# Kernel optimization log

Hardware: AMD Instinct MI355X
Metric: run time of the kernel (lower is better)

The kernel has to match this reference:

```python
import jax, jax.numpy as jnp
import numpy as np

B = 32768
F = 256
H1 = 16
H2 = 8

def setup_inputs() -> dict:
    key = jax.random.key(0)
    ks = jax.random.split(key, 9)
    x = jax.random.normal(ks[0], (B, F), dtype=jnp.float32)
    # Stacked per-feature MLP params (one UnivariateNetwork per feature)
    W1 = jax.random.normal(ks[1], (F, H1), dtype=jnp.float32) * (1.0 / np.sqrt(1))
    b1 = jax.random.normal(ks[2], (F, H1), dtype=jnp.float32) * 0.05
    W2 = jax.random.normal(ks[3], (F, H1, H2), dtype=jnp.float32) * (1.0 / np.sqrt(H1))
    b2 = jax.random.normal(ks[4], (F, H2), dtype=jnp.float32) * 0.05
    W3 = jax.random.normal(ks[5], (F, H2), dtype=jnp.float32) * (1.0 / np.sqrt(H2))
    b3 = jax.random.normal(ks[6], (F,), dtype=jnp.float32) * 0.05
    theta = jax.random.uniform(ks[7], (F,), dtype=jnp.float32) * 0.05
    bias = jnp.zeros((1,), dtype=jnp.float32)
    return {"x": x, "W1": W1, "b1": b1, "W2": W2, "b2": b2,
            "W3": W3, "b3": b3, "theta": theta, "bias": bias}

def reference(x, W1, b1, W2, b2, W3, b3, theta, bias):
    # Batched per-feature MLP: 1 -> H1 -> H2 -> 1 with ELU, all features at once.
    h1 = jax.nn.elu(x[:, :, None] * W1[None, :, :] + b1[None, :, :])      # [B, F, H1]
    h2 = jax.nn.elu(jnp.einsum('bfh,fhk->bfk', h1, W2) + b2[None, :, :])  # [B, F, H2]
    Z = jnp.einsum('bfk,fk->bf', h2, W3) + b3[None, :]                    # [B, F]
    weights = jax.nn.softplus(theta)                                      # [F]
    y_pred = Z @ weights + bias                                           # [B]
    return (y_pred, weights, Z)
```

## Files before the change

kernel.cpp:

```cpp
#include <hip/hip_runtime.h>

#define NB 32768
#define NF 256
#define H1 16
#define H2 8
#define FG 16
#define RJ 4
#define ROWS_PER_BLOCK (16 * RJ)

__device__ __forceinline__ float elu_f(float v) {
    return v > 0.0f ? v : (__expf(v) - 1.0f);
}

__global__ __launch_bounds__(256)
void nul_init(const float* __restrict__ theta, const float* __restrict__ bias,
              float* __restrict__ y_out, float* __restrict__ w_out) {
    const int t = blockIdx.x * 256 + threadIdx.x;
    if (t < NB) y_out[t] = bias[0];
    if (t < NF) w_out[t] = __logf(1.0f + __expf(theta[t]));
}

__global__ __launch_bounds__(256)
void nul_main(const float* __restrict__ x,
              const float* __restrict__ W1, const float* __restrict__ b1,
              const float* __restrict__ W2, const float* __restrict__ b2,
              const float* __restrict__ W3, const float* __restrict__ b3,
              const float* __restrict__ theta,
              float* __restrict__ y_out, float* __restrict__ z_out) {
    __shared__ __align__(16) float sW1[FG][17];
    __shared__ __align__(16) float sB1[FG][17];
    __shared__ __align__(16) float sW2[FG][132];
    __shared__ __align__(16) float sB2[FG][12];
    __shared__ __align__(16) float sW3[FG][12];
    __shared__ float sB3[FG];
    __shared__ float sWv[FG];

    const int tid  = threadIdx.x;
    const int f0   = blockIdx.y * FG;
    const int row0 = blockIdx.x * ROWS_PER_BLOCK;

    {
        const int f = tid >> 4, h = tid & 15;
        sW1[f][h] = W1[(f0 + f) * H1 + h];
        sB1[f][h] = b1[(f0 + f) * H1 + h];
    }
    {
        const int e = tid * 8;
        const int ff = e >> 7, c = e & 127;
        const float4* p = reinterpret_cast<const float4*>(W2 + (f0 + ff) * (H1 * H2) + c);
        float4 v0 = p[0], v1 = p[1];
        float* d = &sW2[ff][c];
        d[0] = v0.x; d[1] = v0.y; d[2] = v0.z; d[3] = v0.w;
        d[4] = v1.x; d[5] = v1.y; d[6] = v1.z; d[7] = v1.w;
    }
    if (tid < FG * H2) {
        const int f = tid >> 3, k = tid & 7;
        sB2[f][k] = b2[(f0 + f) * H2 + k];
        sW3[f][k] = W3[(f0 + f) * H2 + k];
    }
    if (tid < FG) {
        sB3[tid] = b3[f0 + tid];
        sWv[tid] = __logf(1.0f + __expf(theta[f0 + tid]));
    }
    __syncthreads();

    const int fl = tid & 15;
    const int rl = tid >> 4;
    const int f  = f0 + fl;

    float xv[RJ];
    #pragma unroll
    for (int j = 0; j < RJ; ++j)
        xv[j] = x[(row0 + rl + 16 * j) * NF + f];

    float acc[RJ][H2];
    {
        const float4 ba = *reinterpret_cast<const float4*>(&sB2[fl][0]);
        const float4 bb = *reinterpret_cast<const float4*>(&sB2[fl][4]);
        #pragma unroll
        for (int j = 0; j < RJ; ++j) {
            acc[j][0] = ba.x; acc[j][1] = ba.y; acc[j][2] = ba.z; acc[j][3] = ba.w;
            acc[j][4] = bb.x; acc[j][5] = bb.y; acc[j][6] = bb.z; acc[j][7] = bb.w;
        }
    }

    #pragma unroll
    for (int hq = 0; hq < H1 / 4; ++hq) {
        const float4 w1q = *reinterpret_cast<const float4*>(&sW1[fl][hq * 4]);
        const float4 b1q = *reinterpret_cast<const float4*>(&sB1[fl][hq * 4]);
        const float w1a[4] = {w1q.x, w1q.y, w1q.z, w1q.w};
        const float b1a[4] = {b1q.x, b1q.y, b1q.z, b1q.w};
        #pragma unroll
        for (int hh = 0; hh < 4; ++hh) {
            const int h = hq * 4 + hh;
            const float4 wa = *reinterpret_cast<const float4*>(&sW2[fl][h * 8]);
            const float4 wb = *reinterpret_cast<const float4*>(&sW2[fl][h * 8 + 4]);
            #pragma unroll
            for (int j = 0; j < RJ; ++j) {
                const float h1 = elu_f(fmaf(xv[j], w1a[hh], b1a[hh]));
                acc[j][0] = fmaf(h1, wa.x, acc[j][0]);
                acc[j][1] = fmaf(h1, wa.y, acc[j][1]);
                acc[j][2] = fmaf(h1, wa.z, acc[j][2]);
                acc[j][3] = fmaf(h1, wa.w, acc[j][3]);
                acc[j][4] = fmaf(h1, wb.x, acc[j][4]);
                acc[j][5] = fmaf(h1, wb.y, acc[j][5]);
                acc[j][6] = fmaf(h1, wb.z, acc[j][6]);
                acc[j][7] = fmaf(h1, wb.w, acc[j][7]);
            }
        }
    }

    const float4 w3a = *reinterpret_cast<const float4*>(&sW3[fl][0]);
    const float4 w3b = *reinterpret_cast<const float4*>(&sW3[fl][4]);
    const float  b3v = sB3[fl];
    const float  wv  = sWv[fl];

    #pragma unroll
    for (int j = 0; j < RJ; ++j) {
        float z = b3v;
        z = fmaf(elu_f(acc[j][0]), w3a.x, z);
        z = fmaf(elu_f(acc[j][1]), w3a.y, z);
        z = fmaf(elu_f(acc[j][2]), w3a.z, z);
        z = fmaf(elu_f(acc[j][3]), w3a.w, z);
        z = fmaf(elu_f(acc[j][4]), w3b.x, z);
        z = fmaf(elu_f(acc[j][5]), w3b.y, z);
        z = fmaf(elu_f(acc[j][6]), w3b.z, z);
        z = fmaf(elu_f(acc[j][7]), w3b.w, z);

        const int row = row0 + rl + 16 * j;
        z_out[row * NF + f] = z;

        float p = wv * z;
        p += __shfl_xor(p, 1, 16);
        p += __shfl_xor(p, 2, 16);
        p += __shfl_xor(p, 4, 16);
        p += __shfl_xor(p, 8, 16);
        if (fl == 0) unsafeAtomicAdd(&y_out[row], p);
    }
}

extern "C" void kernel_launch(void* const* d_in, const int* in_sizes, int n_in,
                              void* d_out, int out_size, void* d_ws, size_t ws_size,
                              hipStream_t stream) {
    const float* x     = (const float*)d_in[0];
    const float* W1    = (const float*)d_in[1];
    const float* b1    = (const float*)d_in[2];
    const float* W2    = (const float*)d_in[3];
    const float* b2    = (const float*)d_in[4];
    const float* W3    = (const float*)d_in[5];
    const float* b3    = (const float*)d_in[6];
    const float* theta = (const float*)d_in[7];
    const float* bias  = (const float*)d_in[8];

    float* y_out = (float*)d_out;
    float* w_out = y_out + NB;
    float* z_out = w_out + NF;

    nul_init<<<NB / 256, 256, 0, stream>>>(theta, bias, y_out, w_out);

    dim3 grid(NB / ROWS_PER_BLOCK, NF / FG);
    nul_main<<<grid, 256, 0, stream>>>(
        x, W1, b1, W2, b2, W3, b3, theta, y_out, z_out);
}
```

Before: 161.4 us.

## Loop row chunks per block with x prefetch and ds_swizzle reductions

Each block now walks four chunks of 128 rows instead of handling 64 rows once. The x values for the next chunk are prefetched while the current chunk computes. This spreads the shared-memory weight staging over more rows and hides global-load latency. It doubles rows per thread per chunk, raising register pressure, and cuts the grid size by 8x. The shuffle-xor reduction is replaced with ds_swizzle xor patterns within 16-lane groups.

```diff
diff --git a/kernel.cpp b/kernel.cpp
--- a/kernel.cpp
+++ b/kernel.cpp
@@ -5,11 +5,18 @@
 #define H1 16
 #define H2 8
 #define FG 16
-#define RJ 4
-#define ROWS_PER_BLOCK (16 * RJ)
+#define RJ 8
+#define RT 4
+#define ROWS_PER_CHUNK (16 * RJ)
+#define ROWS_PER_BLOCK (ROWS_PER_CHUNK * RT)
 
 __device__ __forceinline__ float elu_f(float v) {
     return v > 0.0f ? v : (__expf(v) - 1.0f);
+}
+
+template <int PAT>
+__device__ __forceinline__ float swz_add(float p) {
+    return p + __int_as_float(__builtin_amdgcn_ds_swizzle(__float_as_int(p), PAT));
 }
 
 __global__ __launch_bounds__(256)
@@ -68,74 +75,90 @@
     const int rl = tid >> 4;
     const int f  = f0 + fl;
 
+    const float4 ba  = *reinterpret_cast<const float4*>(&sB2[fl][0]);
+    const float4 bb  = *reinterpret_cast<const float4*>(&sB2[fl][4]);
+    const float4 w3a = *reinterpret_cast<const float4*>(&sW3[fl][0]);
+    const float4 w3b = *reinterpret_cast<const float4*>(&sW3[fl][4]);
+    const float  b3v = sB3[fl];
+    const float  wv  = sWv[fl];
+    const float* xcol = x + f;
+
     float xv[RJ];
     #pragma unroll
     for (int j = 0; j < RJ; ++j)
-        xv[j] = x[(row0 + rl + 16 * j) * NF + f];
+        xv[j] = xcol[(row0 + rl + 16 * j) * NF];
 
-    float acc[RJ][H2];
-    {
-        const float4 ba = *reinterpret_cast<const float4*>(&sB2[fl][0]);
-        const float4 bb = *reinterpret_cast<const float4*>(&sB2[fl][4]);
+    #pragma unroll 1
+    for (int c = 0; c < RT; ++c) {
+        const int rbase = row0 + c * ROWS_PER_CHUNK;
+
+        float xn[RJ];
+        if (c + 1 < RT) {
+            #pragma unroll
+            for (int j = 0; j < RJ; ++j)
+                xn[j] = xcol[(rbase + ROWS_PER_CHUNK + rl + 16 * j) * NF];
+        }
+
+        float acc[RJ][H2];
         #pragma unroll
         for (int j = 0; j < RJ; ++j) {
             acc[j][0] = ba.x; acc[j][1] = ba.y; acc[j][2] = ba.z; acc[j][3] = ba.w;
             acc[j][4] = bb.x; acc[j][5] = bb.y; acc[j][6] = bb.z; acc[j][7] = bb.w;
         }
-    }
 
-    #pragma unroll
-    for (int hq = 0; hq < H1 / 4; ++hq) {
-        const float4 w1q = *reinterpret_cast<const float4*>(&sW1[fl][hq * 4]);
-        const float4 b1q = *reinterpret_cast<const float4*>(&sB1[fl][hq * 4]);
-        const float w1a[4] = {w1q.x, w1q.y, w1q.z, w1q.w};
-        const float b1a[4] = {b1q.x, b1q.y, b1q.z, b1q.w};
         #pragma unroll
-        for (int hh = 0; hh < 4; ++hh) {
-            const int h = hq * 4 + hh;
-            const float4 wa = *reinterpret_cast<const float4*>(&sW2[fl][h * 8]);
-            const float4 wb = *reinterpret_cast<const float4*>(&sW2[fl][h * 8 + 4]);
+        for (int hq = 0; hq < H1 / 4; ++hq) {
+            const float4 w1q = *reinterpret_cast<const float4*>(&sW1[fl][hq * 4]);
+            const float4 b1q = *reinterpret_cast<const float4*>(&sB1[fl][hq * 4]);
+            const float w1a[4] = {w1q.x, w1q.y, w1q.z, w1q.w};
+            const float b1a[4] = {b1q.x, b1q.y, b1q.z, b1q.w};
             #pragma unroll
-            for (int j = 0; j < RJ; ++j) {
-                const float h1 = elu_f(fmaf(xv[j], w1a[hh], b1a[hh]));
-                acc[j][0] = fmaf(h1, wa.x, acc[j][0]);
-                acc[j][1] = fmaf(h1, wa.y, acc[j][1]);
-                acc[j][2] = fmaf(h1, wa.z, acc[j][2]);
-                acc[j][3] = fmaf(h1, wa.w, acc[j][3]);
-                acc[j][4] = fmaf(h1, wb.x, acc[j][4]);
-                acc[j][5] = fmaf(h1, wb.y, acc[j][5]);
-                acc[j][6] = fmaf(h1, wb.z, acc[j][6]);
-                acc[j][7] = fmaf(h1, wb.w, acc[j][7]);
+            for (int hh = 0; hh < 4; ++hh) {
+                const int h = hq * 4 + hh;
+                const float4 wa = *reinterpret_cast<const float4*>(&sW2[fl][h * 8]);
+                const float4 wb = *reinterpret_cast<const float4*>(&sW2[fl][h * 8 + 4]);
+                #pragma unroll
+                for (int j = 0; j < RJ; ++j) {
+                    const float h1 = elu_f(fmaf(xv[j], w1a[hh], b1a[hh]));
+                    acc[j][0] = fmaf(h1, wa.x, acc[j][0]);
+                    acc[j][1] = fmaf(h1, wa.y, acc[j][1]);
+                    acc[j][2] = fmaf(h1, wa.z, acc[j][2]);
+                    acc[j][3] = fmaf(h1, wa.w, acc[j][3]);
+                    acc[j][4] = fmaf(h1, wb.x, acc[j][4]);
+                    acc[j][5] = fmaf(h1, wb.y, acc[j][5]);
+                    acc[j][6] = fmaf(h1, wb.z, acc[j][6]);
+                    acc[j][7] = fmaf(h1, wb.w, acc[j][7]);
+                }
             }
         }
-    }
 
-    const float4 w3a = *reinterpret_cast<const float4*>(&sW3[fl][0]);
-    const float4 w3b = *reinterpret_cast<const float4*>(&sW3[fl][4]);
-    const float  b3v = sB3[fl];
-    const float  wv  = sWv[fl];
+        #pragma unroll
+        for (int j = 0; j < RJ; ++j) {
+            float z = b3v;
+            z = fmaf(elu_f(acc[j][0]), w3a.x, z);
+            z = fmaf(elu_f(acc[j][1]), w3a.y, z);
+            z = fmaf(elu_f(acc[j][2]), w3a.z, z);
+            z = fmaf(elu_f(acc[j][3]), w3a.w, z);
+            z = fmaf(elu_f(acc[j][4]), w3b.x, z);
+            z = fmaf(elu_f(acc[j][5]), w3b.y, z);
+            z = fmaf(elu_f(acc[j][6]), w3b.z, z);
+            z = fmaf(elu_f(acc[j][7]), w3b.w, z);
 
-    #pragma unroll
-    for (int j = 0; j < RJ; ++j) {
-        float z = b3v;
-        z = fmaf(elu_f(acc[j][0]), w3a.x, z);
-        z = fmaf(elu_f(acc[j][1]), w3a.y, z);
-        z = fmaf(elu_f(acc[j][2]), w3a.z, z);
-        z = fmaf(elu_f(acc[j][3]), w3a.w, z);
-        z = fmaf(elu_f(acc[j][4]), w3b.x, z);
-        z = fmaf(elu_f(acc[j][5]), w3b.y, z);
-        z = fmaf(elu_f(acc[j][6]), w3b.z, z);
-        z = fmaf(elu_f(acc[j][7]), w3b.w, z);
+            const int row = rbase + rl + 16 * j;
+            z_out[row * NF + f] = z;
 
-        const int row = row0 + rl + 16 * j;
-        z_out[row * NF + f] = z;
+            float p = wv * z;
+            p = swz_add<0x041F>(p);
+            p = swz_add<0x081F>(p);
+            p = swz_add<0x101F>(p);
+            p = swz_add<0x201F>(p);
+            if (fl == 0) unsafeAtomicAdd(&y_out[row], p);
+        }
 
-        float p = wv * z;
-        p += __shfl_xor(p, 1, 16);
-        p += __shfl_xor(p, 2, 16);
-        p += __shfl_xor(p, 4, 16);
-        p += __shfl_xor(p, 8, 16);
-        if (fl == 0) unsafeAtomicAdd(&y_out[row], p);
+        if (c + 1 < RT) {
+            #pragma unroll
+            for (int j = 0; j < RJ; ++j) xv[j] = xn[j];
+        }
     }
 }
 
```

Result: faster. 149.4 us (-7.4%).
